# Kernel tuning notes

Hardware: AMD Instinct MI355X
Metric: run time of the kernel (lower is better)

## Reference

```python
import jax, jax.numpy as jnp
import numpy as np

# ---- static config ----
SCALES = [1, 2, 3, 4, 6, 9, 13, 19, 27, 40, 60, 88, 128]
L = sum(SCALES)            # 400
FIRST_L = SCALES[0]        # 1
C = 1024                   # emb_dim (C == D)
DEPTH = 8
H = 16
DH = C // H
CVAE = 64
V = 4096
ND = 256                   # node_embed_size
MLP = 4 * C
B = 32
EPS = 1e-6

_LVL = np.concatenate([np.full(pn, i, dtype=np.int32) for i, pn in enumerate(SCALES)])  # [L]
_BIAS = np.where(_LVL[:, None] >= _LVL[None, :], 0.0, -np.inf).astype(np.float32)        # [L,L]


def _ln(x):
    # LayerNorm without affine params (VAR's ln_wo_grad), eps=1e-6
    m = jnp.mean(x, axis=-1, keepdims=True)
    v = jnp.mean(jnp.square(x - m), axis=-1, keepdims=True)
    return (x - m) * jax.lax.rsqrt(v + EPS)


def setup_inputs() -> dict:
    key = jax.random.key(0)
    ks = iter(jax.random.split(key, 40))
    def p(shape, s=0.02):
        return jax.random.normal(next(ks), shape, dtype=jnp.float32) * s
    inp = {
        "x_BLCv_wo_first_l": jax.random.normal(next(ks), (B, L - FIRST_L, CVAE), jnp.float32),
        "poc_context": jax.random.normal(next(ks), (B, L, CVAE), jnp.float32),
        "poc_cond": jax.random.normal(next(ks), (B, ND), jnp.float32),
        # embedders / positional
        "word_w": p((CVAE, C)), "word_b": p((C,)),
        "poc_w": p((ND, C)), "poc_b": p((C,)),
        "pos_start": p((1, FIRST_L, C)),
        "pos_1LC": p((1, L, C)),
        "lvl_tab": p((len(SCALES), C)),
        # shared AdaLN (SiLU -> Linear(D, 6C))
        "ada_w": p((C, 6 * C)), "ada_b": p((6 * C,)),
        # per-block params, stacked over depth
        "ada_gss": p((DEPTH, 1, 1, 6, C)),
        "q_w": p((DEPTH, C, C)), "q_b": p((DEPTH, C)),
        "kv_w": p((DEPTH, C, 2 * C)), "kv_b": p((DEPTH, 2 * C)),
        "proj_w": p((DEPTH, C, C)), "proj_b": p((DEPTH, C)),
        "fc1_w": p((DEPTH, C, MLP)), "fc1_b": p((DEPTH, MLP)),
        "fc2_w": p((DEPTH, MLP, C)), "fc2_b": p((DEPTH, C)),
        # AdaLNBeforeHead (SiLU -> Linear(D, 2C)) + head
        "head_ada_w": p((C, 2 * C)), "head_ada_b": p((2 * C,)),
        "head_w": p((C, V)), "head_b": p((V,)),
    }
    return inp


def reference(x_BLCv_wo_first_l, poc_context, poc_cond,
              word_w, word_b, poc_w, poc_b, pos_start, pos_1LC, lvl_tab,
              ada_w, ada_b, ada_gss, q_w, q_b, kv_w, kv_b, proj_w, proj_b,
              fc1_w, fc1_b, fc2_w, fc2_b, head_ada_w, head_ada_b, head_w, head_b):
    lvl_idx = jnp.asarray(_LVL)
    bias = jnp.asarray(_BIAS)                      # [L,L] block scale-causal
    scale = 1.0 / np.sqrt(DH)

    cond = poc_cond @ poc_w + poc_b                # [B,C] (cond_BD == sos source)
    sos = cond[:, None, :] + pos_start             # [B,first_l,C]
    x = jnp.concatenate([sos, x_BLCv_wo_first_l @ word_w + word_b], axis=1)  # [B,L,C]
    lvl = lvl_tab[lvl_idx] + pos_1LC[0]            # [L,C]
    x = x + lvl
    poc = (poc_context @ word_w + word_b) + lvl    # [B,L,C]

    gss = jax.nn.silu(cond) @ ada_w + ada_b        # [B,6C]
    gss = gss.reshape(B, 1, 6, C)

    def block(x, params):
        ag, qw, qb, kvw, kvb, pw, pb, f1w, f1b, f2w, f2b = params
        mod = ag + gss                             # [B,1,6,C]
        g1, g2, s1, s2, sh1, sh2 = [mod[:, :, i] for i in range(6)]  # each [B,1,C]
        # cross-attention (q from modulated x, kv from poc context), scale-causal bias
        xn = _ln(x) * (1.0 + s1) + sh1
        q = (xn @ qw + qb).reshape(B, L, H, DH)
        kv = (poc @ kvw + kvb).reshape(B, L, 2, H, DH)
        k, v = kv[:, :, 0], kv[:, :, 1]
        att = jnp.einsum('bqhd,bkhd->bhqk', q, k) * scale + bias
        att = jax.nn.softmax(att, axis=-1)
        o = jnp.einsum('bhqk,bkhd->bqhd', att, v).reshape(B, L, C)
        x = x + g1 * (o @ pw + pb)
        # FFN with AdaLN modulation
        xn2 = _ln(x) * (1.0 + s2) + sh2
        hdn = jax.nn.gelu(xn2 @ f1w + f1b, approximate=False)
        x = x + g2 * (hdn @ f2w + f2b)
        return x, None

    x, _ = jax.lax.scan(block, x, (ada_gss, q_w, q_b, kv_w, kv_b, proj_w, proj_b,
                                   fc1_w, fc1_b, fc2_w, fc2_b))

    # AdaLNBeforeHead + head
    ss = jax.nn.silu(cond) @ head_ada_w + head_ada_b   # [B,2C]
    h_scale, h_shift = ss[:, None, :C], ss[:, None, C:]
    x = _ln(x) * (1.0 + h_scale) + h_shift
    logits = x @ head_w + head_b                       # [B,L,V]
    return logits
```

## Files before the change

### kernel.cpp

```cpp
#include <hip/hip_runtime.h>
#include <hip/hip_bf16.h>
#include <math.h>

#define DEV __device__ __forceinline__

typedef __attribute__((ext_vector_type(4))) float f32x4;
typedef __attribute__((ext_vector_type(8))) short bf16x8;
typedef __attribute__((ext_vector_type(4))) short s16x4;

static constexpr int Bz = 32, Lz = 400, Cz = 1024, MLPz = 4096;
static constexpr int BL = Bz * Lz;

DEV float bf2f(unsigned short u) {
  union { unsigned int i; float f; } v; v.i = ((unsigned int)u) << 16; return v.f;
}
DEV unsigned short f2bf(float f) {
  union { float f; unsigned int i; } v; v.f = f;
  unsigned int r = v.i + 0x7FFFu + ((v.i >> 16) & 1u);
  return (unsigned short)(r >> 16);
}

DEV int level_of(int l) {
  const int cum[13] = {1,3,6,10,16,25,38,57,84,124,184,272,400};
  int lv = 12;
  #pragma unroll
  for (int i = 12; i >= 0; i--) if (l < cum[i]) lv = i;
  return lv;
}
DEV int row_kmax(int l) {
  const int cum[13] = {1,3,6,10,16,25,38,57,84,124,184,272,400};
  int km = 400;
  #pragma unroll
  for (int i = 12; i >= 0; i--) if (l < cum[i]) km = cum[i];
  return km;
}

DEV void stage16(const unsigned short* g, unsigned short* l) {
#if __has_builtin(__builtin_amdgcn_global_load_lds)
  __builtin_amdgcn_global_load_lds((const __attribute__((address_space(1))) void*)g,
                                   (__attribute__((address_space(3))) void*)l, 16, 0, 0);
#else
  *(bf16x8*)l = *(const bf16x8*)g;
#endif
}

__global__ __launch_bounds__(256)
void tconv_k(const float* __restrict__ in, unsigned short* __restrict__ out, int K, int N)
{
  __shared__ float t[64][65];
  const int n0 = blockIdx.x * 64, k0 = blockIdx.y * 64;
  #pragma unroll
  for (int i = 0; i < 16; i++) {
    int idx = i * 256 + threadIdx.x;
    int r = idx >> 6, c = idx & 63;
    t[r][c] = in[(size_t)(k0 + r) * N + n0 + c];
  }
  __syncthreads();
  #pragma unroll
  for (int i = 0; i < 16; i++) {
    int idx = i * 256 + threadIdx.x;
    int rn = idx >> 6, ck = idx & 63;
    out[(size_t)(n0 + rn) * K + k0 + ck] = f2bf(t[ck][rn]);
  }
}

enum { EP_BF16 = 0, EP_GELU = 1, EP_RESID = 2, EP_F32 = 3, EP_KV = 4 };

template<int MODE>
__global__ __launch_bounds__(256, 2)
void gemm2_k(const unsigned short* __restrict__ A, const unsigned short* __restrict__ Bt,
             const float* __restrict__ bias, void* __restrict__ out,
             float* __restrict__ xres, const float* __restrict__ gsh,
             const float* __restrict__ gpb, unsigned short* __restrict__ vtb,
             int N, int K)
{
  __shared__ unsigned short As[128 * 64];
  __shared__ unsigned short Bs[128 * 64];
  const int tid = threadIdx.x;
  const int lane = tid & 63, wv = tid >> 6;
  const int row0 = blockIdx.x * 128, col0 = blockIdx.y * 128;
  const int wm = (wv >> 1) * 64, wn = (wv & 1) * 64;

  f32x4 acc[4][4] = {};

  for (int k0 = 0; k0 < K; k0 += 64) {
    #pragma unroll
    for (int i = 0; i < 4; i++) {
      int ch = i * 256 + tid;
      int r = ch >> 3;
      int c8 = (ch & 7) ^ (r & 7);
      stage16(A + (size_t)(row0 + r) * K + k0 + c8 * 8, As + ch * 8);
    }
    #pragma unroll
    for (int i = 0; i < 4; i++) {
      int ch = i * 256 + tid;
      int r = ch >> 3;
      int c8 = (ch & 7) ^ (r & 7);
      stage16(Bt + (size_t)(col0 + r) * K + k0 + c8 * 8, Bs + ch * 8);
    }
    __syncthreads();
    #pragma unroll
    for (int kk = 0; kk < 2; kk++) {
      bf16x8 af[4], bfr[4];
      const int bcol = kk * 64 + (lane >> 4) * 16;
      #pragma unroll
      for (int m = 0; m < 4; m++) {
        int r = wm + m * 16 + (lane & 15);
        af[m] = *(const bf16x8*)((char*)As + r * 128 + (bcol ^ ((r & 7) << 4)));
      }
      #pragma unroll
      for (int n = 0; n < 4; n++) {
        int r = wn + n * 16 + (lane & 15);
        bfr[n] = *(const bf16x8*)((char*)Bs + r * 128 + (bcol ^ ((r & 7) << 4)));
      }
      #pragma unroll
      for (int m = 0; m < 4; m++)
        #pragma unroll
        for (int n = 0; n < 4; n++)
          acc[m][n] = __builtin_amdgcn_mfma_f32_16x16x32_bf16(af[m], bfr[n], acc[m][n], 0, 0, 0);
    }
    __syncthreads();
  }

  const int rbase = row0 + wm + ((lane >> 4) << 2);
  const int cbase = col0 + wn + (lane & 15);
  #pragma unroll
  for (int n = 0; n < 4; n++) {
    int gcol = cbase + n * 16;
    float bv = bias[gcol];
    #pragma unroll
    for (int m = 0; m < 4; m++) {
      #pragma unroll
      for (int r = 0; r < 4; r++) {
        int grow = rbase + m * 16 + r;
        float v = acc[m][n][r] + bv;
        if constexpr (MODE == EP_BF16) {
          ((unsigned short*)out)[(size_t)grow * N + gcol] = f2bf(v);
        } else if constexpr (MODE == EP_GELU) {
          float g = 0.5f * v * (1.f + erff(v * 0.70710678118654752f));
          ((unsigned short*)out)[(size_t)grow * N + gcol] = f2bf(g);
        } else if constexpr (MODE == EP_RESID) {
          int b = grow / Lz;
          float g = gsh[gcol] + gpb[(size_t)b * 6144 + gcol];
          xres[(size_t)grow * Cz + gcol] += g * v;
        } else if constexpr (MODE == EP_KV) {
          if (gcol < 1024) {
            ((unsigned short*)out)[(size_t)grow * 1024 + gcol] = f2bf(v);
          } else {
            int b = grow / Lz, l = grow - b * Lz;
            int h = (gcol >> 6) & 15, d = gcol & 63;
            vtb[(((size_t)b * 16 + h) * 64 + d) * Lz + l] = f2bf(v);
          }
        } else {
          ((float*)out)[(size_t)grow * N + gcol] = v;
        }
      }
    }
  }
}

__global__ __launch_bounds__(256)
void ln_k(const float* __restrict__ x, unsigned short* __restrict__ out,
          const float* __restrict__ ssh, const float* __restrict__ spb, int sstride,
          const float* __restrict__ hsh, const float* __restrict__ hpb, int hstride)
{
  const int row = blockIdx.x, tid = threadIdx.x;
  const int b = row / Lz;
  const float* xr = x + (size_t)row * Cz;
  float v[4];
  float s = 0.f;
  #pragma unroll
  for (int i = 0; i < 4; i++) { v[i] = xr[tid + i * 256]; s += v[i]; }
  __shared__ float red[8];
  #pragma unroll
  for (int o = 32; o > 0; o >>= 1) s += __shfl_xor(s, o, 64);
  if ((tid & 63) == 0) red[tid >> 6] = s;
  __syncthreads();
  float mean = (red[0] + red[1] + red[2] + red[3]) * (1.f / 1024.f);
  float vs = 0.f;
  #pragma unroll
  for (int i = 0; i < 4; i++) { float d = v[i] - mean; vs += d * d; }
  #pragma unroll
  for (int o = 32; o > 0; o >>= 1) vs += __shfl_xor(vs, o, 64);
  __syncthreads();
  if ((tid & 63) == 0) red[4 + (tid >> 6)] = vs;
  __syncthreads();
  float var = (red[4] + red[5] + red[6] + red[7]) * (1.f / 1024.f);
  float rstd = rsqrtf(var + 1e-6f);
  #pragma unroll
  for (int i = 0; i < 4; i++) {
    int c = tid + i * 256;
    float sc = (ssh ? ssh[c] : 0.f) + spb[(size_t)b * sstride + c];
    float sh = (hsh ? hsh[c] : 0.f) + hpb[(size_t)b * hstride + c];
    out[(size_t)row * Cz + c] = f2bf((v[i] - mean) * rstd * (1.f + sc) + sh);
  }
}

__global__ __launch_bounds__(512)
void attn3_k(const unsigned short* __restrict__ qb,
             const unsigned short* __restrict__ kbuf,
             const unsigned short* __restrict__ vtb,
             unsigned short* __restrict__ ob)
{
  __shared__ unsigned short Ks[400 * 64];
  __shared__ unsigned short Vt[64 * 408];
  __shared__ unsigned short Pl[8][512];
  const int bh = blockIdx.x, b = bh >> 4, h = bh & 15;
  const int qc = blockIdx.y;
  const int tid = threadIdx.x;
  const int q0 = qc * 128;
  const int nch = (row_kmax(min(q0 + 127, Lz - 1)) + 15) >> 4;

  const size_t kbase = (size_t)b * Lz * 1024 + h * 64;
  for (int i = tid; i < nch * 128; i += 512) {
    int l = i >> 3, d8 = i & 7;
    bf16x8 kr = *(const bf16x8*)&kbuf[kbase + (size_t)l * 1024 + d8 * 8];
    *(bf16x8*)((char*)Ks + l * 128 + ((d8 * 16) ^ ((l & 7) << 4))) = kr;
  }
  const size_t vbase = ((size_t)b * 16 + h) * 64 * Lz;
  for (int i = tid; i < 64 * 50; i += 512) {
    int d = i / 50, c8 = i - d * 50;
    *(bf16x8*)((char*)Vt + d * 816 + c8 * 16) = *(const bf16x8*)&vtb[vbase + (size_t)d * Lz + c8 * 8];
  }
  __syncthreads();

  const int wv = tid >> 6, lane = tid & 63, g = lane >> 4, q = lane & 15;
  const int qw0 = q0 + wv * 16;
  if (qw0 >= Lz) return;
  const int qrow = qw0 + q;
  const int my_kmax = row_kmax(qrow);
  const int nsch = (row_kmax(qw0 + 15) + 31) >> 5;

  const unsigned short* qp = qb + (size_t)(b * Lz + qrow) * Cz + h * 64;
  bf16x8 qf0 = *(const bf16x8*)(qp + g * 8);
  bf16x8 qf1 = *(const bf16x8*)(qp + 32 + g * 8);
  unsigned short* myP = &Pl[wv][0];

  float m = -1e30f, lsum = 0.f;
  f32x4 acc[4] = {};

  for (int sc = 0; sc < nsch; ++sc) {
    f32x4 st0 = {0.f,0.f,0.f,0.f}, st1 = {0.f,0.f,0.f,0.f};
    {
      int kr = sc * 32 + q;
      const char* kb = (const char*)Ks + kr * 128;
      int sw = (kr & 7) << 4;
      bf16x8 k0 = *(const bf16x8*)(kb + ((g * 16) ^ sw));
      bf16x8 k1 = *(const bf16x8*)(kb + ((64 + g * 16) ^ sw));
      st0 = __builtin_amdgcn_mfma_f32_16x16x32_bf16(k0, qf0, st0, 0, 0, 0);
      st0 = __builtin_amdgcn_mfma_f32_16x16x32_bf16(k1, qf1, st0, 0, 0, 0);
    }
    {
      int kr = sc * 32 + 16 + q;
      const char* kb = (const char*)Ks + kr * 128;
      int sw = (kr & 7) << 4;
      bf16x8 k0 = *(const bf16x8*)(kb + ((g * 16) ^ sw));
      bf16x8 k1 = *(const bf16x8*)(kb + ((64 + g * 16) ^ sw));
      st1 = __builtin_amdgcn_mfma_f32_16x16x32_bf16(k0, qf0, st1, 0, 0, 0);
      st1 = __builtin_amdgcn_mfma_f32_16x16x32_bf16(k1, qf1, st1, 0, 0, 0);
    }

    float s8[8]; float cmax = -1e30f;
    #pragma unroll
    for (int r = 0; r < 4; r++) {
      int k0g = sc * 32 + 4 * g + r;
      int k1g = k0g + 16;
      s8[r]     = (k0g < my_kmax) ? st0[r] * 0.125f : -1e30f;
      s8[4 + r] = (k1g < my_kmax) ? st1[r] * 0.125f : -1e30f;
      cmax = fmaxf(cmax, fmaxf(s8[r], s8[4 + r]));
    }
    cmax = fmaxf(cmax, __shfl_xor(cmax, 16, 64));
    cmax = fmaxf(cmax, __shfl_xor(cmax, 32, 64));
    float mnew = fmaxf(m, cmax);
    float f = __expf(m - mnew);
    float p[8], ps = 0.f;
    #pragma unroll
    for (int r = 0; r < 8; r++) { p[r] = __expf(s8[r] - mnew); ps += p[r]; }
    ps += __shfl_xor(ps, 16, 64);
    ps += __shfl_xor(ps, 32, 64);
    lsum = lsum * f + ps;
    m = mnew;
    #pragma unroll
    for (int blk = 0; blk < 4; blk++)
      #pragma unroll
      for (int j = 0; j < 4; j++) acc[blk][j] *= f;

    #pragma unroll
    for (int cp = 0; cp < 2; cp++) {
      #pragma unroll
      for (int j = 0; j < 2; j++) {
        unsigned int lo = f2bf(p[4 * cp + 2 * j]);
        unsigned int hi = f2bf(p[4 * cp + 2 * j + 1]);
        int w = 8 * cp + 2 * g + j;
        *(unsigned int*)((char*)myP + q * 64 + 4 * (w ^ q)) = lo | (hi << 16);
      }
    }

    unsigned int pw[4];
    #pragma unroll
    for (int i = 0; i < 4; i++)
      pw[i] = *(const unsigned int*)((const char*)myP + q * 64 + 4 * ((4 * g + i) ^ q));
    bf16x8 pfrag;
    #pragma unroll
    for (int i = 0; i < 4; i++) {
      pfrag[2 * i]     = (short)(pw[i] & 0xFFFF);
      pfrag[2 * i + 1] = (short)(pw[i] >> 16);
    }

    #pragma unroll
    for (int blk = 0; blk < 4; blk++) {
      bf16x8 vf = *(const bf16x8*)((const char*)Vt + (16 * blk + q) * 816 + (sc * 32 + 8 * g) * 2);
      acc[blk] = __builtin_amdgcn_mfma_f32_16x16x32_bf16(vf, pfrag, acc[blk], 0, 0, 0);
    }
  }

  float inv = 1.f / lsum;
  unsigned short* op = ob + (size_t)(b * Lz + qrow) * Cz + h * 64;
  #pragma unroll
  for (int blk = 0; blk < 4; blk++)
    #pragma unroll
    for (int r = 0; r < 4; r++)
      op[16 * blk + 4 * g + r] = f2bf(acc[blk][r] * inv);
}

__global__ __launch_bounds__(256)
void cond_k(const float* __restrict__ pc, const float* __restrict__ pw,
            const float* __restrict__ pb, float* __restrict__ cond,
            float* __restrict__ silu)
{
  const int b = blockIdx.y;
  const int n = blockIdx.x * 256 + threadIdx.x;
  __shared__ float a[256];
  a[threadIdx.x] = pc[b * 256 + threadIdx.x];
  __syncthreads();
  float s = pb[n];
  for (int k = 0; k < 256; k++) s += a[k] * pw[(size_t)k * Cz + n];
  cond[(size_t)b * Cz + n] = s;
  silu[(size_t)b * Cz + n] = s / (1.f + __expf(-s));
}

__global__ __launch_bounds__(256)
void smallmm_k(const float* __restrict__ A, const float* __restrict__ W,
               const float* __restrict__ bias, float* __restrict__ out, int N)
{
  const int b = blockIdx.y;
  const int n = blockIdx.x * 256 + threadIdx.x;
  __shared__ float a[1024];
  for (int i = threadIdx.x; i < 1024; i += 256) a[i] = A[(size_t)b * 1024 + i];
  __syncthreads();
  float s = bias[n];
  for (int k = 0; k < 1024; k++) s += a[k] * W[(size_t)k * N + n];
  out[(size_t)b * N + n] = s;
}

template<int MODE>
__global__ __launch_bounds__(256)
void embed_k(const float* __restrict__ src, const float* __restrict__ ww,
             const float* __restrict__ wb, const float* __restrict__ cond,
             const float* __restrict__ pos_start, const float* __restrict__ pos1,
             const float* __restrict__ ltab, void* __restrict__ out)
{
  const int r0 = blockIdx.x * 4;
  const int tid = threadIdx.x;
  const int b = r0 / Lz;
  __shared__ float a[4][64];
  {
    int rr = tid >> 6, k = tid & 63;
    int l = (r0 + rr) % Lz;
    float val;
    if (MODE == 0) val = (l == 0) ? 0.f : src[((size_t)b * (Lz - 1) + (l - 1)) * 64 + k];
    else           val = src[((size_t)(r0 + rr)) * 64 + k];
    a[rr][k] = val;
  }
  __syncthreads();
  #pragma unroll
  for (int ci = 0; ci < 4; ci++) {
    int c = tid + ci * 256;
    float s[4];
    #pragma unroll
    for (int rr = 0; rr < 4; rr++) {
      int l = (r0 + rr) % Lz;
      s[rr] = wb[c] + ltab[(size_t)level_of(l) * Cz + c] + pos1[(size_t)l * Cz + c];
    }
    for (int k = 0; k < 64; k++) {
      float w = ww[(size_t)k * Cz + c];
      #pragma unroll
      for (int rr = 0; rr < 4; rr++) s[rr] += a[rr][k] * w;
    }
    #pragma unroll
    for (int rr = 0; rr < 4; rr++) {
      int l = (r0 + rr) % Lz;
      if (MODE == 0) {
        float val = s[rr];
        if (l == 0) val = cond[(size_t)b * Cz + c] + pos_start[c] + ltab[c] + pos1[c];
        ((float*)out)[((size_t)(r0 + rr)) * Cz + c] = val;
      } else {
        ((unsigned short*)out)[((size_t)(r0 + rr)) * Cz + c] = f2bf(s[rr]);
      }
    }
  }
}

extern "C" void kernel_launch(void* const* d_in, const int* in_sizes, int n_in,
                              void* d_out, int out_size, void* d_ws, size_t ws_size,
                              hipStream_t stream)
{
  (void)in_sizes; (void)n_in; (void)out_size; (void)ws_size;
  const float* x_blcv   = (const float*)d_in[0];
  const float* poc_ctx  = (const float*)d_in[1];
  const float* poc_cond = (const float*)d_in[2];
  const float* word_w   = (const float*)d_in[3];
  const float* word_b   = (const float*)d_in[4];
  const float* poc_w    = (const float*)d_in[5];
  const float* poc_b    = (const float*)d_in[6];
  const float* pos_start= (const float*)d_in[7];
  const float* pos_1lc  = (const float*)d_in[8];
  const float* lvl_tab  = (const float*)d_in[9];
  const float* ada_w    = (const float*)d_in[10];
  const float* ada_b    = (const float*)d_in[11];
  const float* ada_gss  = (const float*)d_in[12];
  const float* q_w      = (const float*)d_in[13];
  const float* q_b      = (const float*)d_in[14];
  const float* kv_w     = (const float*)d_in[15];
  const float* kv_b     = (const float*)d_in[16];
  const float* proj_w   = (const float*)d_in[17];
  const float* proj_b   = (const float*)d_in[18];
  const float* fc1_w    = (const float*)d_in[19];
  const float* fc1_b    = (const float*)d_in[20];
  const float* fc2_w    = (const float*)d_in[21];
  const float* fc2_b    = (const float*)d_in[22];
  const float* head_ada_w = (const float*)d_in[23];
  const float* head_ada_b = (const float*)d_in[24];
  const float* head_w   = (const float*)d_in[25];
  const float* head_b   = (const float*)d_in[26];

  char* p = (char*)d_ws;
  auto carve = [&](size_t bytes) { void* r = (void*)p; p += (bytes + 255) & ~(size_t)255; return r; };
  float* x            = (float*)carve((size_t)BL * Cz * 4);
  unsigned short* xn  = (unsigned short*)carve((size_t)BL * Cz * 2);
  unsigned short* poc = (unsigned short*)carve((size_t)BL * Cz * 2);
  unsigned short* qbf = (unsigned short*)carve((size_t)BL * Cz * 2);
  unsigned short* kbuf= (unsigned short*)carve((size_t)BL * Cz * 2);
  unsigned short* vtb = (unsigned short*)carve((size_t)BL * Cz * 2);
  unsigned short* ob  = (unsigned short*)carve((size_t)BL * Cz * 2);
  unsigned short* hdn = (unsigned short*)carve((size_t)BL * MLPz * 2);
  unsigned short* wt  = (unsigned short*)carve((size_t)12582912 * 2);
  float* cond  = (float*)carve(32 * 1024 * 4);
  float* siluc = (float*)carve(32 * 1024 * 4);
  float* gss   = (float*)carve(32 * 6144 * 4);
  float* ss    = (float*)carve(32 * 2048 * 4);

  unsigned short* qwt  = wt;
  unsigned short* kvwt = wt + 1048576;
  unsigned short* pjwt = wt + 3145728;
  unsigned short* f1wt = wt + 4194304;
  unsigned short* f2wt = wt + 8388608;

  cond_k<<<dim3(4, 32), 256, 0, stream>>>(poc_cond, poc_w, poc_b, cond, siluc);
  smallmm_k<<<dim3(24, 32), 256, 0, stream>>>(siluc, ada_w, ada_b, gss, 6144);
  smallmm_k<<<dim3(8, 32), 256, 0, stream>>>(siluc, head_ada_w, head_ada_b, ss, 2048);
  embed_k<0><<<3200, 256, 0, stream>>>(x_blcv, word_w, word_b, cond, pos_start, pos_1lc, lvl_tab, x);
  embed_k<1><<<3200, 256, 0, stream>>>(poc_ctx, word_w, word_b, cond, pos_start, pos_1lc, lvl_tab, poc);

  for (int d = 0; d < 8; d++) {
    const float* ag = ada_gss + (size_t)d * 6144;
    tconv_k<<<dim3(16, 16), 256, 0, stream>>>(q_w + (size_t)d * 1048576, qwt, 1024, 1024);
    tconv_k<<<dim3(32, 16), 256, 0, stream>>>(kv_w + (size_t)d * 2097152, kvwt, 1024, 2048);
    tconv_k<<<dim3(16, 16), 256, 0, stream>>>(proj_w + (size_t)d * 1048576, pjwt, 1024, 1024);
    tconv_k<<<dim3(64, 16), 256, 0, stream>>>(fc1_w + (size_t)d * 4194304, f1wt, 1024, 4096);
    tconv_k<<<dim3(16, 64), 256, 0, stream>>>(fc2_w + (size_t)d * 4194304, f2wt, 4096, 1024);

    ln_k<<<BL, 256, 0, stream>>>(x, xn, ag + 2 * 1024, gss + 2 * 1024, 6144,
                                 ag + 4 * 1024, gss + 4 * 1024, 6144);
    gemm2_k<EP_BF16><<<dim3(100, 8), 256, 0, stream>>>(
        xn, qwt, q_b + d * 1024, qbf, nullptr, nullptr, nullptr, nullptr, 1024, 1024);
    gemm2_k<EP_KV><<<dim3(100, 16), 256, 0, stream>>>(
        poc, kvwt, kv_b + d * 2048, kbuf, nullptr, nullptr, nullptr, vtb, 2048, 1024);
    attn3_k<<<dim3(512, 4), 512, 0, stream>>>(qbf, kbuf, vtb, ob);
    gemm2_k<EP_RESID><<<dim3(100, 8), 256, 0, stream>>>(
        ob, pjwt, proj_b + d * 1024, nullptr, x, ag + 0, gss + 0, nullptr, 1024, 1024);
    ln_k<<<BL, 256, 0, stream>>>(x, xn, ag + 3 * 1024, gss + 3 * 1024, 6144,
                                 ag + 5 * 1024, gss + 5 * 1024, 6144);
    gemm2_k<EP_GELU><<<dim3(100, 32), 256, 0, stream>>>(
        xn, f1wt, fc1_b + d * 4096, hdn, nullptr, nullptr, nullptr, nullptr, 4096, 1024);
    gemm2_k<EP_RESID><<<dim3(100, 8), 256, 0, stream>>>(
        hdn, f2wt, fc2_b + d * 1024, nullptr, x, ag + 1024, gss + 1024, nullptr, 1024, 4096);
  }
  ln_k<<<BL, 256, 0, stream>>>(x, xn, nullptr, ss, 2048, nullptr, ss + 1024, 2048);
  tconv_k<<<dim3(64, 16), 256, 0, stream>>>(head_w, wt, 1024, 4096);
  gemm2_k<EP_F32><<<dim3(100, 32), 256, 0, stream>>>(
      xn, wt, head_b, d_out, nullptr, nullptr, nullptr, nullptr, 4096, 1024);
}
```

Before: 6.115 ms.

## Replace GEMM with 256x256 8-wave double-buffered pipelined kernel

Replaces the 128x128 four-wave GEMM with a 256x256 tile, eight-wave kernel. It double-buffers A and B in 128KB of LDS and interleaves the global-to-LDS staging of the next K tiles with the MFMA work on the current ones, using explicit vmcnt waits, barriers and setprio. It also swizzles the block index so neighbouring workgroups share tiles, and raises per-block data reuse. The risks are lower occupancy from the large LDS footprint and more register pressure. It also assumes M=12800 splits into 50 row tiles and that the grid size is divisible by 8.

```diff
diff --git a/kernel.cpp b/kernel.cpp
--- a/kernel.cpp
+++ b/kernel.cpp
@@ -66,74 +66,146 @@
 
 enum { EP_BF16 = 0, EP_GELU = 1, EP_RESID = 2, EP_F32 = 3, EP_KV = 4 };
 
+#define G8_VMCNT4() asm volatile("s_waitcnt vmcnt(4)" ::: "memory")
+#define G8_VMCNT0() asm volatile("s_waitcnt vmcnt(0)" ::: "memory")
+#define G8_SYNC1() do { __builtin_amdgcn_s_barrier(); \
+  asm volatile("s_waitcnt lgkmcnt(0)" ::: "memory"); \
+  __builtin_amdgcn_sched_barrier(0); } while (0)
+#define G8_SYNC1N() __builtin_amdgcn_s_barrier()
+#define G8_END() __builtin_amdgcn_s_barrier()
+
+#define G8_READA(buf, mh) do { \
+  const char* base_ = (const char*)lds + (buf) * 32768 + wm * 16384; \
+  _Pragma("unroll") \
+  for (int mfi = 0; mfi < 4; mfi++) { \
+    int rl = (mh) * 64 + mfi * 16 + (lane & 15); \
+    int sw = (rl & 7) << 4; \
+    _Pragma("unroll") \
+    for (int kk = 0; kk < 2; kk++) \
+      af[mfi][kk] = *(const bf16x8*)(base_ + rl * 128 + ((kk * 64 + (lane >> 4) * 16) ^ sw)); \
+  } \
+} while (0)
+
+#define G8_READB(buf, nh, bfz) do { \
+  const char* base_ = (const char*)lds + 65536 + (buf) * 32768 + (wn >> 1) * 16384; \
+  _Pragma("unroll") \
+  for (int nfi = 0; nfi < 2; nfi++) { \
+    int rl = (wn & 1) * 64 + (nh) * 32 + nfi * 16 + (lane & 15); \
+    int sw = (rl & 7) << 4; \
+    _Pragma("unroll") \
+    for (int kk = 0; kk < 2; kk++) \
+      bfz[nfi][kk] = *(const bf16x8*)(base_ + rl * 128 + ((kk * 64 + (lane >> 4) * 16) ^ sw)); \
+  } \
+} while (0)
+
+#define G8_MFMA(mh, nh, bfz) do { \
+  __builtin_amdgcn_s_setprio(1); \
+  _Pragma("unroll") \
+  for (int mfi = 0; mfi < 4; mfi++) \
+    _Pragma("unroll") \
+    for (int nfi = 0; nfi < 2; nfi++) \
+      _Pragma("unroll") \
+      for (int kk = 0; kk < 2; kk++) \
+        acc[(mh) * 4 + mfi][(nh) * 2 + nfi] = __builtin_amdgcn_mfma_f32_16x16x32_bf16( \
+            af[mfi][kk], bfz[nfi][kk], acc[(mh) * 4 + mfi][(nh) * 2 + nfi], 0, 0, 0); \
+  __builtin_amdgcn_s_setprio(0); \
+} while (0)
+
+#define G8_STAGEA(buf, h, t) do { \
+  unsigned short* dst_ = lds + (buf) * 16384 + (h) * 8192; \
+  const unsigned short* src_ = A + (size_t)(row0 + (h) * 128) * K + (t) * 64; \
+  _Pragma("unroll") \
+  for (int i_ = 0; i_ < 2; i_++) { \
+    int ch_ = i_ * 512 + tid; \
+    int r_ = ch_ >> 3, c8_ = (ch_ & 7) ^ (r_ & 7); \
+    stage16(src_ + (size_t)r_ * K + c8_ * 8, dst_ + ch_ * 8); \
+  } \
+} while (0)
+
+#define G8_STAGEB(buf, h, t) do { \
+  unsigned short* dst_ = lds + 32768 + (buf) * 16384 + (h) * 8192; \
+  const unsigned short* src_ = Bt + (size_t)(col0 + (h) * 128) * K + (t) * 64; \
+  _Pragma("unroll") \
+  for (int i_ = 0; i_ < 2; i_++) { \
+    int ch_ = i_ * 512 + tid; \
+    int r_ = ch_ >> 3, c8_ = (ch_ & 7) ^ (r_ & 7); \
+    stage16(src_ + (size_t)r_ * K + c8_ * 8, dst_ + ch_ * 8); \
+  } \
+} while (0)
+
 template<int MODE>
-__global__ __launch_bounds__(256, 2)
-void gemm2_k(const unsigned short* __restrict__ A, const unsigned short* __restrict__ Bt,
+__global__ __launch_bounds__(512, 2)
+void gemm8_k(const unsigned short* __restrict__ A, const unsigned short* __restrict__ Bt,
              const float* __restrict__ bias, void* __restrict__ out,
              float* __restrict__ xres, const float* __restrict__ gsh,
              const float* __restrict__ gpb, unsigned short* __restrict__ vtb,
              int N, int K)
 {
-  __shared__ unsigned short As[128 * 64];
-  __shared__ unsigned short Bs[128 * 64];
+  __shared__ unsigned short lds[65536];
   const int tid = threadIdx.x;
-  const int lane = tid & 63, wv = tid >> 6;
-  const int row0 = blockIdx.x * 128, col0 = blockIdx.y * 128;
-  const int wm = (wv >> 1) * 64, wn = (wv & 1) * 64;
-
-  f32x4 acc[4][4] = {};
-
-  for (int k0 = 0; k0 < K; k0 += 64) {
-    #pragma unroll
-    for (int i = 0; i < 4; i++) {
-      int ch = i * 256 + tid;
-      int r = ch >> 3;
-      int c8 = (ch & 7) ^ (r & 7);
-      stage16(A + (size_t)(row0 + r) * K + k0 + c8 * 8, As + ch * 8);
-    }
-    #pragma unroll
-    for (int i = 0; i < 4; i++) {
-      int ch = i * 256 + tid;
-      int r = ch >> 3;
-      int c8 = (ch & 7) ^ (r & 7);
-      stage16(Bt + (size_t)(col0 + r) * K + k0 + c8 * 8, Bs + ch * 8);
-    }
-    __syncthreads();
-    #pragma unroll
-    for (int kk = 0; kk < 2; kk++) {
-      bf16x8 af[4], bfr[4];
-      const int bcol = kk * 64 + (lane >> 4) * 16;
-      #pragma unroll
-      for (int m = 0; m < 4; m++) {
-        int r = wm + m * 16 + (lane & 15);
-        af[m] = *(const bf16x8*)((char*)As + r * 128 + (bcol ^ ((r & 7) << 4)));
-      }
-      #pragma unroll
-      for (int n = 0; n < 4; n++) {
-        int r = wn + n * 16 + (lane & 15);
-        bfr[n] = *(const bf16x8*)((char*)Bs + r * 128 + (bcol ^ ((r & 7) << 4)));
-      }
-      #pragma unroll
-      for (int m = 0; m < 4; m++)
-        #pragma unroll
-        for (int n = 0; n < 4; n++)
-          acc[m][n] = __builtin_amdgcn_mfma_f32_16x16x32_bf16(af[m], bfr[n], acc[m][n], 0, 0, 0);
-    }
-    __syncthreads();
-  }
-
-  const int rbase = row0 + wm + ((lane >> 4) << 2);
-  const int cbase = col0 + wn + (lane & 15);
-  #pragma unroll
-  for (int n = 0; n < 4; n++) {
-    int gcol = cbase + n * 16;
+  const int lane = tid & 63;
+  const int wid = tid >> 6;
+  const int wm = wid >> 2;
+  const int wn = wid & 3;
+
+  const int nwg = gridDim.x;
+  const int cpx = nwg >> 3;
+  const int swz = (blockIdx.x & 7) * cpx + (blockIdx.x >> 3);
+  const int row0 = (swz % 50) * 256;
+  const int col0 = (swz / 50) * 256;
+
+  bf16x8 af[4][2], b0f[2][2], b1f[2][2];
+  f32x4 acc[8][4] = {};
+
+  const int NT = K >> 6;
+  const int NIT = NT >> 1;
+
+  G8_STAGEA(0, 0, 0); G8_STAGEA(0, 1, 0);
+  G8_STAGEB(0, 0, 0); G8_STAGEB(0, 1, 0);
+  G8_STAGEB(1, 0, 1); G8_STAGEB(1, 1, 1);
+  G8_VMCNT4();
+  __builtin_amdgcn_s_barrier();
+
+  for (int it = 0; it < NIT; ++it) {
+    const int ta = 2 * it, tb = ta + 1;
+    const bool last = (it == NIT - 1);
+    G8_READA(0, 0); G8_READB(0, 0, b0f);
+    G8_STAGEA(1, 0, tb);
+    G8_SYNC1(); G8_MFMA(0, 0, b0f); G8_END();
+    G8_READB(0, 1, b1f);
+    G8_STAGEA(1, 1, tb);
+    G8_SYNC1(); G8_MFMA(0, 1, b1f); G8_END();
+    G8_READA(0, 1);
+    if (!last) G8_STAGEB(0, 0, ta + 2);
+    G8_SYNC1(); G8_MFMA(1, 1, b1f); G8_END();
+    if (!last) { G8_STAGEB(0, 1, ta + 2); G8_VMCNT4(); }
+    else       { G8_VMCNT0(); }
+    G8_SYNC1N(); G8_MFMA(1, 0, b0f); G8_END();
+    G8_READA(1, 0); G8_READB(1, 0, b0f);
+    if (!last) G8_STAGEA(0, 0, ta + 2);
+    G8_SYNC1(); G8_MFMA(0, 0, b0f); G8_END();
+    G8_READB(1, 1, b1f);
+    if (!last) G8_STAGEA(0, 1, ta + 2);
+    G8_SYNC1(); G8_MFMA(0, 1, b1f); G8_END();
+    G8_READA(1, 1);
+    if (!last) G8_STAGEB(1, 0, tb + 2);
+    G8_SYNC1(); G8_MFMA(1, 1, b1f); G8_END();
+    if (!last) { G8_STAGEB(1, 1, tb + 2); G8_VMCNT4(); }
+    G8_SYNC1N(); G8_MFMA(1, 0, b0f); G8_END();
+  }
+
+  const int rbase = row0 + wm * 128 + ((lane >> 4) << 2);
+  const int cbase = col0 + wn * 64 + (lane & 15);
+  #pragma unroll
+  for (int nf = 0; nf < 4; nf++) {
+    int gcol = cbase + nf * 16;
     float bv = bias[gcol];
     #pragma unroll
-    for (int m = 0; m < 4; m++) {
+    for (int mf = 0; mf < 8; mf++) {
       #pragma unroll
       for (int r = 0; r < 4; r++) {
-        int grow = rbase + m * 16 + r;
-        float v = acc[m][n][r] + bv;
+        int grow = rbase + mf * 16 + r;
+        float v = acc[mf][nf][r] + bv;
         if constexpr (MODE == EP_BF16) {
           ((unsigned short*)out)[(size_t)grow * N + gcol] = f2bf(v);
         } else if constexpr (MODE == EP_GELU) {
@@ -472,22 +544,22 @@
 
     ln_k<<<BL, 256, 0, stream>>>(x, xn, ag + 2 * 1024, gss + 2 * 1024, 6144,
                                  ag + 4 * 1024, gss + 4 * 1024, 6144);
-    gemm2_k<EP_BF16><<<dim3(100, 8), 256, 0, stream>>>(
+    gemm8_k<EP_BF16><<<200, 512, 0, stream>>>(
         xn, qwt, q_b + d * 1024, qbf, nullptr, nullptr, nullptr, nullptr, 1024, 1024);
-    gemm2_k<EP_KV><<<dim3(100, 16), 256, 0, stream>>>(
+    gemm8_k<EP_KV><<<400, 512, 0, stream>>>(
         poc, kvwt, kv_b + d * 2048, kbuf, nullptr, nullptr, nullptr, vtb, 2048, 1024);
     attn3_k<<<dim3(512, 4), 512, 0, stream>>>(qbf, kbuf, vtb, ob);
-    gemm2_k<EP_RESID><<<dim3(100, 8), 256, 0, stream>>>(
+    gemm8_k<EP_RESID><<<200, 512, 0, stream>>>(
         ob, pjwt, proj_b + d * 1024, nullptr, x, ag + 0, gss + 0, nullptr, 1024, 1024);
     ln_k<<<BL, 256, 0, stream>>>(x, xn, ag + 3 * 1024, gss + 3 * 1024, 6144,
                                  ag + 5 * 1024, gss + 5 * 1024, 6144);
-    gemm2_k<EP_GELU><<<dim3(100, 32), 256, 0, stream>>>(
+    gemm8_k<EP_GELU><<<800, 512, 0, stream>>>(
         xn, f1wt, fc1_b + d * 4096, hdn, nullptr, nullptr, nullptr, nullptr, 4096, 1024);
-    gemm2_k<EP_RESID><<<dim3(100, 8), 256, 0, stream>>>(
+    gemm8_k<EP_RESID><<<200, 512, 0, stream>>>(
         hdn, f2wt, fc2_b + d * 1024, nullptr, x, ag + 1024, gss + 1024, nullptr, 1024, 4096);
   }
   ln_k<<<BL, 256, 0, stream>>>(x, xn, nullptr, ss, 2048, nullptr, ss + 1024, 2048);
   tconv_k<<<dim3(64, 16), 256, 0, stream>>>(head_w, wt, 1024, 4096);
-  gemm2_k<EP_F32><<<dim3(100, 32), 256, 0, stream>>>(
+  gemm8_k<EP_F32><<<800, 512, 0, stream>>>(
       xn, wt, head_b, d_out, nullptr, nullptr, nullptr, nullptr, 4096, 1024);
 }
```

New measurement: 6.281 ms. +2.7%, slower.
